# Kernel tuning notes

Hardware: AMD Instinct MI355X
Metric: run time of the kernel (lower is better)

Reference implementation:

```python
import jax, jax.numpy as jnp
import numpy as np

N_S, N_D, E, L = 10000, 2000, 100000, 50000
H = 8            # attention heads
H1, H2, H3 = 128, 128, 64
D_S, D_D = 128, 64
NEG_SLOPE = 0.2  # GATv2 leaky_relu slope


def setup_inputs() -> dict:
    key = jax.random.key(0)
    ks = iter(jax.random.split(key, 48))
    def nrm(shape, fan_in):
        return (jax.random.normal(next(ks), shape) / np.sqrt(fan_in)).astype(jnp.float32)
    inp = {}
    inp["x_snorna"] = jax.random.normal(next(ks), (N_S, D_S), dtype=jnp.float32)
    inp["x_disease"] = jax.random.normal(next(ks), (N_D, D_D), dtype=jnp.float32)
    inp["edge_src"] = jax.random.randint(next(ks), (E,), 0, N_S, dtype=jnp.int32)
    inp["edge_dst"] = jax.random.randint(next(ks), (E,), 0, N_D, dtype=jnp.int32)
    inp["edge_label_src"] = jax.random.randint(next(ks), (L,), 0, N_S, dtype=jnp.int32)
    inp["edge_label_dst"] = jax.random.randint(next(ks), (L,), 0, N_D, dtype=jnp.int32)
    # layer 1: GraphConv per relation (lin_rel has bias, lin_root no bias)
    inp["W1_rel_sd"] = nrm((D_S, H1), D_S); inp["b1_sd"] = jnp.zeros((H1,), jnp.float32)
    inp["W1_root_sd"] = nrm((D_D, H1), D_D)
    inp["W1_rel_ds"] = nrm((D_D, H1), D_D); inp["b1_ds"] = jnp.zeros((H1,), jnp.float32)
    inp["W1_root_ds"] = nrm((D_S, H1), D_S)
    # layer 2: GATv2Conv per relation (lin_l/lin_r with bias, att, final bias)
    for rel in ("sd", "ds"):
        inp[f"Wl2_{rel}"] = nrm((H1, H * H2), H1); inp[f"bl2_{rel}"] = jnp.zeros((H * H2,), jnp.float32)
        inp[f"Wr2_{rel}"] = nrm((H1, H * H2), H1); inp[f"br2_{rel}"] = jnp.zeros((H * H2,), jnp.float32)
        inp[f"att2_{rel}"] = nrm((H, H2), H2)
        inp[f"bias2_{rel}"] = jnp.zeros((H2,), jnp.float32)
    # layer 3: GraphConv per relation
    inp["W3_rel_sd"] = nrm((H2, H3), H2); inp["b3_sd"] = jnp.zeros((H3,), jnp.float32)
    inp["W3_root_sd"] = nrm((H2, H3), H2)
    inp["W3_rel_ds"] = nrm((H2, H3), H2); inp["b3_ds"] = jnp.zeros((H3,), jnp.float32)
    inp["W3_root_ds"] = nrm((H2, H3), H2)
    return inp


def graph_conv(x_src, x_dst, es, ed, W_rel, b_rel, W_root, n_dst):
    # PyG GraphConv: lin_rel(sum-aggregated neighbor feats) + lin_root(x_dst)
    agg = jax.ops.segment_sum(x_src[es], ed, num_segments=n_dst)
    return agg @ W_rel + b_rel + x_dst @ W_root


def gatv2(x_src, x_dst, es, ed, Wl, bl, Wr, br, att, bias, n_dst):
    # PyG GATv2Conv, bipartite, add_self_loops=False, concat=False (mean over heads)
    xl = (x_src @ Wl + bl).reshape(x_src.shape[0], H, -1)  # [Ns,H,C]
    xr = (x_dst @ Wr + br).reshape(x_dst.shape[0], H, -1)  # [Nd,H,C]
    xj = xl[es]                                            # [E,H,C] source msgs
    e = jax.nn.leaky_relu(xj + xr[ed], NEG_SLOPE)          # [E,H,C]
    score = jnp.einsum('ehc,hc->eh', e, att)               # [E,H]
    m = jax.ops.segment_max(score, ed, num_segments=n_dst)
    a = jnp.exp(score - m[ed])
    denom = jax.ops.segment_sum(a, ed, num_segments=n_dst)
    alpha = a / denom[ed]                                  # softmax over in-edges of dst
    out = jax.ops.segment_sum(alpha[:, :, None] * xj, ed, num_segments=n_dst)
    return out.mean(axis=1) + bias                         # concat=False -> head mean


def reference(x_snorna, x_disease, edge_src, edge_dst, edge_label_src, edge_label_dst,
              W1_rel_sd, b1_sd, W1_root_sd, W1_rel_ds, b1_ds, W1_root_ds,
              Wl2_sd, bl2_sd, Wr2_sd, br2_sd, att2_sd, bias2_sd,
              Wl2_ds, bl2_ds, Wr2_ds, br2_ds, att2_ds, bias2_ds,
              W3_rel_sd, b3_sd, W3_root_sd, W3_rel_ds, b3_ds, W3_root_ds):
    # HeteroConv layer 1 (GraphConv both directions); each type has one incoming relation
    xd = graph_conv(x_snorna, x_disease, edge_src, edge_dst, W1_rel_sd, b1_sd, W1_root_sd, N_D)
    xs = graph_conv(x_disease, x_snorna, edge_dst, edge_src, W1_rel_ds, b1_ds, W1_root_ds, N_S)
    xs, xd = jax.nn.relu(xs), jax.nn.relu(xd)  # dropout = identity (eval mode)
    # HeteroConv layer 2 (GATv2Conv both directions)
    xd2 = gatv2(xs, xd, edge_src, edge_dst, Wl2_sd, bl2_sd, Wr2_sd, br2_sd, att2_sd, bias2_sd, N_D)
    xs2 = gatv2(xd, xs, edge_dst, edge_src, Wl2_ds, bl2_ds, Wr2_ds, br2_ds, att2_ds, bias2_ds, N_S)
    xs2, xd2 = jax.nn.relu(xs2), jax.nn.relu(xd2)
    # HeteroConv layer 3 (GraphConv, no activation)
    xd3 = graph_conv(xs2, xd2, edge_src, edge_dst, W3_rel_sd, b3_sd, W3_root_sd, N_D)
    xs3 = graph_conv(xd2, xs2, edge_dst, edge_src, W3_rel_ds, b3_ds, W3_root_ds, N_S)
    # Classifier: per-pair dot product
    return (xs3[edge_label_src] * xd3[edge_label_dst]).sum(axis=-1)
```

## Files before the change

### kernel.cpp

```cpp
#include <hip/hip_runtime.h>
#include <math.h>

#define NEG 0.2f
static const int N_S = 10000, N_D = 2000, E_N = 100000, L_N = 50000;

using short8 = __attribute__((ext_vector_type(8))) short;
using f32x4  = __attribute__((ext_vector_type(4))) float;
typedef _Float16 h2 __attribute__((ext_vector_type(2)));

union U8h { uint4 u[2]; h2 h[8]; unsigned w[8]; };

__device__ inline unsigned short f2bf(float f) {
  unsigned u = __float_as_uint(f);
  u += 0x7fff + ((u >> 16) & 1);
  return (unsigned short)(u >> 16);
}
__device__ inline float bf2f(unsigned short u) {
  return __uint_as_float((unsigned)u << 16);
}
__device__ inline unsigned short f2h(float f) {
  _Float16 h = (_Float16)f;
  unsigned short r;
  __builtin_memcpy(&r, &h, 2);
  return r;
}

struct PkD { const float* W; unsigned short* P; int K, M; };
struct Pk12 { PkD d[12]; };
struct PrepArgs {
  const int *es, *ed;
  int *deg_s, *deg_d;
  const float *xs, *xd;
  unsigned short *xsb, *xdb;
  const float *att_sd, *att_ds;
  unsigned short *att16;
};
__global__ void k_prep(PrepArgs a, Pk12 g) {
  int bid = blockIdx.x, t = threadIdx.x;
  if (bid < 391) {
    int e = bid * 256 + t;
    if (e < E_N) {
      atomicAdd(&a.deg_d[a.ed[e]], 1);
      atomicAdd(&a.deg_s[a.es[e]], 1);
    }
  } else if (bid < 391 + 1375) {
    int i = (bid - 391) * 256 + t;
    const int ns4 = N_S * 32;
    if (i < ns4) {
      float4 v = ((const float4*)a.xs)[i];
      ushort4 o = {f2bf(v.x), f2bf(v.y), f2bf(v.z), f2bf(v.w)};
      ((ushort4*)a.xsb)[i] = o;
    } else {
      int j = i - ns4;
      float4 v = ((const float4*)a.xd)[j];
      ushort4 o = {f2bf(v.x), f2bf(v.y), f2bf(v.z), f2bf(v.w)};
      ((ushort4*)a.xdb)[j] = o;
    }
  } else if (bid < 391 + 1375 + 768) {
    int sub = bid - 391 - 1375;
    PkD d = g.d[sub >> 6];
    int total = d.K * d.M, mt = d.M >> 4;
    for (int tid = (sub & 63) * 256 + t; tid < total; tid += 64 * 256) {
      int r = tid & 7, l = (tid >> 3) & 63, rest = tid >> 9;
      int ct = rest % mt, kt = rest / mt;
      d.P[tid] = f2bf(d.W[(kt * 32 + (l >> 4) * 8 + r) * d.M + ct * 16 + (l & 15)]);
    }
  } else {
    int i = (bid - 391 - 1375 - 768) * 256 + t;
    float v = (i < 1024) ? a.att_sd[i] : a.att_ds[i - 1024];
    a.att16[i] = f2h(v);
  }
}

__global__ __launch_bounds__(1024) void k_scan2(int* c0, int* r0, int n0,
                                                int* c1, int* r1, int n1) {
  int* cur = blockIdx.x ? c1 : c0;
  int* rp  = blockIdx.x ? r1 : r0;
  int N    = blockIdx.x ? n1 : n0;
  __shared__ int wsum[16];
  __shared__ int carry;
  if (threadIdx.x == 0) carry = 0;
  __syncthreads();
  int lane = threadIdx.x & 63, wid = threadIdx.x >> 6;
  for (int base = 0; base < N; base += 1024) {
    int i = base + threadIdx.x;
    int v = (i < N) ? cur[i] : 0;
    int x = v;
    #pragma unroll
    for (int dd = 1; dd < 64; dd <<= 1) {
      int t = __shfl_up(x, dd);
      if (lane >= dd) x += t;
    }
    if (lane == 63) wsum[wid] = x;
    __syncthreads();
    int woff = 0;
    for (int ww = 0; ww < wid; ++ww) woff += wsum[ww];
    int excl = carry + woff + x - v;
    if (i < N) { rp[i] = excl; cur[i] = excl; }
    __syncthreads();
    if (threadIdx.x == 0) {
      int t = 0;
      #pragma unroll
      for (int ww = 0; ww < 16; ++ww) t += wsum[ww];
      if (base + 1024 >= N) rp[N] = carry + t;
      carry += t;
    }
    __syncthreads();
  }
}

__global__ void k_scat2(const int* __restrict__ es, const int* __restrict__ ed,
                        int* __restrict__ cur_d, int* __restrict__ cur_s,
                        int* __restrict__ csrc_d, int* __restrict__ csrc_s, int E) {
  int e = blockIdx.x * 256 + threadIdx.x;
  if (e >= E) return;
  int s = es[e], d = ed[e];
  csrc_d[atomicAdd(&cur_d[d], 1)] = s;
  csrc_s[atomicAdd(&cur_s[s], 1)] = d;
}

__device__ __forceinline__ void gath128(const unsigned short* __restrict__ x,
                                        const int* __restrict__ rp, const int* __restrict__ cs,
                                        unsigned short* __restrict__ out,
                                        int n, int half, int cl) {
  int b = rp[n], e = rp[n + 1];
  float a0 = 0.f, a1 = 0.f, a2 = 0.f, a3 = 0.f;
  int i = b + half;
  for (; i + 2 < e; i += 4) {
    uint2 v0 = *(const uint2*)(x + (long long)cs[i] * 128 + cl * 4);
    uint2 v1 = *(const uint2*)(x + (long long)cs[i + 2] * 128 + cl * 4);
    a0 += bf2f((unsigned short)(v0.x & 0xffff)) + bf2f((unsigned short)(v1.x & 0xffff));
    a1 += bf2f((unsigned short)(v0.x >> 16))    + bf2f((unsigned short)(v1.x >> 16));
    a2 += bf2f((unsigned short)(v0.y & 0xffff)) + bf2f((unsigned short)(v1.y & 0xffff));
    a3 += bf2f((unsigned short)(v0.y >> 16))    + bf2f((unsigned short)(v1.y >> 16));
  }
  for (; i < e; i += 2) {
    uint2 v0 = *(const uint2*)(x + (long long)cs[i] * 128 + cl * 4);
    a0 += bf2f((unsigned short)(v0.x & 0xffff));
    a1 += bf2f((unsigned short)(v0.x >> 16));
    a2 += bf2f((unsigned short)(v0.y & 0xffff));
    a3 += bf2f((unsigned short)(v0.y >> 16));
  }
  a0 += __shfl_xor(a0, 32); a1 += __shfl_xor(a1, 32);
  a2 += __shfl_xor(a2, 32); a3 += __shfl_xor(a3, 32);
  if (!half) {
    ushort4 o = {f2bf(a0), f2bf(a1), f2bf(a2), f2bf(a3)};
    *(ushort4*)&out[(long long)n * 128 + cl * 4] = o;
  }
}

__global__ __launch_bounds__(256) void k_gather1(
    const unsigned short* __restrict__ xsb, const unsigned short* __restrict__ xdb,
    const int* __restrict__ rpd, const int* __restrict__ csd,
    const int* __restrict__ rps, const int* __restrict__ css,
    unsigned short* __restrict__ aggd, unsigned short* __restrict__ aggs) {
  int wv = threadIdx.x >> 6, l = threadIdx.x & 63, half = l >> 5, cl = l & 31;
  int r = blockIdx.x % 6, q = blockIdx.x / 6;
  if (r == 0) {
    gath128(xsb, rpd, csd, aggd, q * 4 + wv, half, cl);
  } else {
    int n = (q * 5 + (r - 1)) * 4 + wv;
    if (n >= N_S) return;
    int b = rps[n], e = rps[n + 1];
    float a0 = 0.f, a1 = 0.f;
    int i = b + half;
    for (; i + 2 < e; i += 4) {
      unsigned v0 = *(const unsigned*)(xdb + (long long)css[i] * 64 + cl * 2);
      unsigned v1 = *(const unsigned*)(xdb + (long long)css[i + 2] * 64 + cl * 2);
      a0 += bf2f((unsigned short)(v0 & 0xffff)) + bf2f((unsigned short)(v1 & 0xffff));
      a1 += bf2f((unsigned short)(v0 >> 16))    + bf2f((unsigned short)(v1 >> 16));
    }
    for (; i < e; i += 2) {
      unsigned v0 = *(const unsigned*)(xdb + (long long)css[i] * 64 + cl * 2);
      a0 += bf2f((unsigned short)(v0 & 0xffff));
      a1 += bf2f((unsigned short)(v0 >> 16));
    }
    a0 += __shfl_xor(a0, 32); a1 += __shfl_xor(a1, 32);
    if (!half) {
      ushort2 o = {f2bf(a0), f2bf(a1)};
      *(ushort2*)&aggs[(long long)n * 64 + cl * 2] = o;
    }
  }
}

__global__ __launch_bounds__(256) void k_gather3(
    const unsigned short* __restrict__ xs2b, const unsigned short* __restrict__ xd2b,
    const int* __restrict__ rpd, const int* __restrict__ csd,
    const int* __restrict__ rps, const int* __restrict__ css,
    unsigned short* __restrict__ aggd, unsigned short* __restrict__ aggs) {
  int wv = threadIdx.x >> 6, l = threadIdx.x & 63, half = l >> 5, cl = l & 31;
  int r = blockIdx.x % 6, q = blockIdx.x / 6;
  if (r == 0) {
    gath128(xs2b, rpd, csd, aggd, q * 4 + wv, half, cl);
  } else {
    int n = (q * 5 + (r - 1)) * 4 + wv;
    if (n >= N_S) return;
    gath128(xd2b, rps, css, aggs, n, half, cl);
  }
}

struct GD {
  const unsigned short *A0, *P0, *A1, *P1;
  const float* bias;
  void* out;
  int K0, K1, N, M, relu, outmode, y0;
};
template<int ND> struct GDs { GD d[ND]; };

template<int ND>
__global__ __launch_bounds__(256) void k_mfma(GDs<ND> g) {
  int by = blockIdx.y;
  int di = 0;
  #pragma unroll
  for (int i = 1; i < ND; ++i) if (by >= g.d[i].y0) di = i;
  GD d = g.d[di];
  int ytile = by - d.y0;
  int c0 = blockIdx.x * 64;
  if (c0 >= d.M) return;
  int w = threadIdx.x >> 6, l = threadIdx.x & 63;
  int r0 = ytile * 64 + w * 16;
  if (r0 >= d.N) return;
  int lg = l >> 4, lo = l & 15;
  f32x4 acc[4] = {};
  int arow = r0 + lo; arow = (arow < d.N) ? arow : (d.N - 1);
  int mt = d.M >> 4;
  int ct0 = c0 >> 4;
  const unsigned short* a0 = d.A0 + (long long)arow * d.K0 + lg * 8;
  for (int kt = 0; kt < (d.K0 >> 5); ++kt) {
    short8 a = *(const short8*)(a0 + kt * 32);
    #pragma unroll
    for (int ct = 0; ct < 4; ++ct) {
      short8 b = *(const short8*)(d.P0 + ((long long)(kt * mt + ct0 + ct) * 64 + l) * 8);
      acc[ct] = __builtin_amdgcn_mfma_f32_16x16x32_bf16(a, b, acc[ct], 0, 0, 0);
    }
  }
  if (d.K1) {
    const unsigned short* a1 = d.A1 + (long long)arow * d.K1 + lg * 8;
    for (int kt = 0; kt < (d.K1 >> 5); ++kt) {
      short8 a = *(const short8*)(a1 + kt * 32);
      #pragma unroll
      for (int ct = 0; ct < 4; ++ct) {
        short8 b = *(const short8*)(d.P1 + ((long long)(kt * mt + ct0 + ct) * 64 + l) * 8);
        acc[ct] = __builtin_amdgcn_mfma_f32_16x16x32_bf16(a, b, acc[ct], 0, 0, 0);
      }
    }
  }
  #pragma unroll
  for (int ct = 0; ct < 4; ++ct) {
    int col = c0 + ct * 16 + lo;
    float bv = d.bias[col];
    #pragma unroll
    for (int r = 0; r < 4; ++r) {
      int grow = r0 + lg * 4 + r;
      if (grow < d.N) {
        float v = acc[ct][r] + bv;
        if (d.relu) v = fmaxf(v, 0.f);
        if (d.outmode == 1)
          ((unsigned short*)d.out)[(long long)grow * d.M + col] = f2bf(v);
        else if (d.outmode == 2)
          ((unsigned short*)d.out)[(long long)grow * d.M + col] = f2h(v);
        else
          ((float*)d.out)[(long long)grow * d.M + col] = v;
      }
    }
  }
}

template<int WPN>
__device__ __forceinline__ void gat_node(
    const unsigned short* __restrict__ xl, const unsigned short* __restrict__ xr,
    const int* __restrict__ rowptr, const int* __restrict__ srcid,
    const unsigned short* __restrict__ att16, const float* __restrict__ bias,
    unsigned short* __restrict__ outb, int node, int wsub, int l,
    float (*lm)[8], float (*lss)[8], unsigned (*lacc)[8][64]) {
  int h = l >> 3, sub = l & 7;
  int cbase = h * 128 + sub * 16;
  U8h xr8, at8;
  { const uint4* p = (const uint4*)(xr + (long long)node * 1024 + cbase);
    xr8.u[0] = p[0]; xr8.u[1] = p[1]; }
  { const uint4* p = (const uint4*)(att16 + cbase);
    at8.u[0] = p[0]; at8.u[1] = p[1]; }
  const h2 neg2 = {(_Float16)NEG, (_Float16)NEG};
  float m = -INFINITY, s = 0.f;
  h2 acc2[8] = {};
  int b = rowptr[node], e = rowptr[node + 1];
  int deg = e - b;

  auto ldrow = [&](int idx, U8h& dst) {
    int ic = idx < e - 1 ? idx : e - 1;
    ic = ic > 0 ? ic : 0;
    const uint4* p = (const uint4*)(xl + (long long)srcid[ic] * 1024 + cbase);
    dst.u[0] = p[0]; dst.u[1] = p[1];
  };

  auto process = [&](U8h& x, bool valid) {
    float sc = 0.f;
    #pragma unroll
    for (int j = 0; j < 8; ++j) {
      h2 t = x.h[j] + xr8.h[j];
      h2 lk = __builtin_elementwise_max(t, t * neg2);
      sc = __builtin_amdgcn_fdot2(lk, at8.h[j], sc, false);
    }
    sc += __shfl_xor(sc, 1); sc += __shfl_xor(sc, 2); sc += __shfl_xor(sc, 4);
    if (valid && sc > m + 4.f) {
      float scl = __expf(m - sc);
      _Float16 sh = (_Float16)scl;
      h2 s2 = {sh, sh};
      #pragma unroll
      for (int j = 0; j < 8; ++j) acc2[j] *= s2;
      s *= scl; m = sc;
    }
    float a = __expf(sc - m);
    a = valid ? a : 0.f;
    s += a;
    _Float16 ah = (_Float16)(a * 0.00390625f);
    h2 a2 = {ah, ah};
    #pragma unroll
    for (int j = 0; j < 8; ++j) acc2[j] = __builtin_elementwise_fma(a2, x.h[j], acc2[j]);
  };

  int i = b + wsub;
  int nmine = (deg - wsub + WPN - 1) / WPN;
  if (nmine < 0) nmine = 0;
  int npairs = (nmine + 1) >> 1;
  U8h c, d;
  ldrow(i, c);
  ldrow(i + WPN, d);
  for (int it = 0; it < npairs; ++it) {
    int j = i + 2 * WPN;
    U8h n0, n1;
    ldrow(j, n0);
    ldrow(j + WPN, n1);
    process(c, i < e);
    process(d, i + WPN < e);
    c = n0; d = n1; i = j;
  }

  float val[16];
  if constexpr (WPN == 4) {
    if (sub == 0) { lm[wsub][h] = m; lss[wsub][h] = s; }
    U8h tmp;
    #pragma unroll
    for (int j = 0; j < 8; ++j) tmp.h[j] = acc2[j];
    #pragma unroll
    for (int j = 0; j < 8; ++j) lacc[wsub][j][l] = tmp.w[j];
    __syncthreads();
    if (wsub != 0) return;
    float M2 = fmaxf(fmaxf(lm[0][h], lm[1][h]), fmaxf(lm[2][h], lm[3][h]));
    float S = 0.f;
    #pragma unroll
    for (int j = 0; j < 16; ++j) val[j] = 0.f;
    #pragma unroll
    for (int w2 = 0; w2 < 4; ++w2) {
      float scw = (M2 == -INFINITY) ? 0.f : __expf(lm[w2][h] - M2);
      S = fmaf(scw, lss[w2][h], S);
      #pragma unroll
      for (int j = 0; j < 8; ++j) {
        unsigned uw = lacc[w2][j][l];
        h2 hv; __builtin_memcpy(&hv, &uw, 4);
        val[2 * j]     = fmaf(scw, (float)hv[0], val[2 * j]);
        val[2 * j + 1] = fmaf(scw, (float)hv[1], val[2 * j + 1]);
      }
    }
    float inv = (S > 0.f) ? 256.f / S : 0.f;
    #pragma unroll
    for (int j = 0; j < 16; ++j) val[j] *= inv;
  } else {
    float inv = (s > 0.f) ? 256.f / s : 0.f;
    #pragma unroll
    for (int j = 0; j < 8; ++j) {
      val[2 * j]     = (float)acc2[j][0] * inv;
      val[2 * j + 1] = (float)acc2[j][1] * inv;
    }
  }
  #pragma unroll
  for (int j = 0; j < 16; ++j) {
    val[j] += __shfl_xor(val[j], 8);
    val[j] += __shfl_xor(val[j], 16);
    val[j] += __shfl_xor(val[j], 32);
  }
  if (l < 8) {
    #pragma unroll
    for (int q = 0; q < 4; ++q) {
      float4 bq = *(const float4*)&bias[sub * 16 + q * 4];
      ushort4 o;
      o.x = f2bf(fmaxf(val[q * 4 + 0] * 0.125f + bq.x, 0.f));
      o.y = f2bf(fmaxf(val[q * 4 + 1] * 0.125f + bq.y, 0.f));
      o.z = f2bf(fmaxf(val[q * 4 + 2] * 0.125f + bq.z, 0.f));
      o.w = f2bf(fmaxf(val[q * 4 + 3] * 0.125f + bq.w, 0.f));
      *(ushort4*)&outb[(long long)node * 128 + sub * 16 + q * 4] = o;
    }
  }
}

__global__ __launch_bounds__(256) void k_gat_both(
    const unsigned short* __restrict__ XLsd, const unsigned short* __restrict__ XRsd,
    const int* __restrict__ rpd, const int* __restrict__ csd,
    const unsigned short* __restrict__ att_sd, const float* __restrict__ bias_sd,
    unsigned short* __restrict__ XD2b,
    const unsigned short* __restrict__ XLds, const unsigned short* __restrict__ XRds,
    const int* __restrict__ rps, const int* __restrict__ css,
    const unsigned short* __restrict__ att_ds, const float* __restrict__ bias_ds,
    unsigned short* __restrict__ XS2b) {
  __shared__ float lm[4][8], lss[4][8];
  __shared__ unsigned lacc[4][8][64];
  int widx = threadIdx.x >> 6, l = threadIdx.x & 63;
  int r = blockIdx.x % 9, q = blockIdx.x / 9;
  if (r < 4) {
    gat_node<4>(XLsd, XRsd, rpd, csd, att_sd, bias_sd, XD2b,
                q * 4 + r, widx, l, lm, lss, lacc);
  } else {
    int node = (q * 5 + (r - 4)) * 4 + widx;
    if (node < N_S)
      gat_node<1>(XLds, XRds, rps, css, att_ds, bias_ds, XS2b,
                  node, 0, l, lm, lss, lacc);
  }
}

__global__ void k_dot64(const float* __restrict__ xs, const float* __restrict__ xd,
                        const int* __restrict__ ls, const int* __restrict__ ld,
                        float* __restrict__ out, int L) {
  long long t = (long long)blockIdx.x * blockDim.x + threadIdx.x;
  int wave = (int)(t >> 6), lane = (int)(t & 63);
  int q = lane >> 4, sub = lane & 15;
  int eidx = wave * 4 + q;
  if (eidx >= L) return;
  const float4* a = (const float4*)(xs + (long long)ls[eidx] * 64);
  const float4* b = (const float4*)(xd + (long long)ld[eidx] * 64);
  float4 va = a[sub], vb = b[sub];
  float v = va.x * vb.x + va.y * vb.y + va.z * vb.z + va.w * vb.w;
  v += __shfl_xor(v, 1); v += __shfl_xor(v, 2);
  v += __shfl_xor(v, 4); v += __shfl_xor(v, 8);
  if (sub == 0) out[eidx] = v;
}

extern "C" void kernel_launch(void* const* d_in, const int* in_sizes, int n_in,
                              void* d_out, int out_size, void* d_ws, size_t ws_size,
                              hipStream_t stream) {
  const float* x_s = (const float*)d_in[0];
  const float* x_d = (const float*)d_in[1];
  const int* esrc = (const int*)d_in[2];
  const int* edst = (const int*)d_in[3];
  const int* lsrc = (const int*)d_in[4];
  const int* ldst = (const int*)d_in[5];
  const float* W1rel_sd  = (const float*)d_in[6];
  const float* b1_sd     = (const float*)d_in[7];
  const float* W1root_sd = (const float*)d_in[8];
  const float* W1rel_ds  = (const float*)d_in[9];
  const float* b1_ds     = (const float*)d_in[10];
  const float* W1root_ds = (const float*)d_in[11];
  const float *Wl2_sd = (const float*)d_in[12], *bl2_sd = (const float*)d_in[13],
              *Wr2_sd = (const float*)d_in[14], *br2_sd = (const float*)d_in[15],
              *att2_sd = (const float*)d_in[16], *bias2_sd = (const float*)d_in[17];
  const float *Wl2_ds = (const float*)d_in[18], *bl2_ds = (const float*)d_in[19],
              *Wr2_ds = (const float*)d_in[20], *br2_ds = (const float*)d_in[21],
              *att2_ds = (const float*)d_in[22], *bias2_ds = (const float*)d_in[23];
  const float *W3rel_sd = (const float*)d_in[24], *b3_sd = (const float*)d_in[25],
              *W3root_sd = (const float*)d_in[26];
  const float *W3rel_ds = (const float*)d_in[27], *b3_ds = (const float*)d_in[28],
              *W3root_ds = (const float*)d_in[29];
  float* out = (float*)d_out;

  float* w = (float*)d_ws;
  long long off = 0;
  auto alloc = [&](long long n) { float* p = w + off; off += (n + 63) & ~63LL; return p; };
  unsigned short* xsb   = (unsigned short*)alloc((long long)N_S * 64);
  unsigned short* xdb   = (unsigned short*)alloc((long long)N_D * 32);
  unsigned short* AGGDb = (unsigned short*)alloc((long long)N_D * 64);
  unsigned short* AGGSb = (unsigned short*)alloc((long long)N_S * 32);
  unsigned short* XS1b  = (unsigned short*)alloc((long long)N_S * 64);
  unsigned short* XD1b  = (unsigned short*)alloc((long long)N_D * 64);
  unsigned short* XLsd  = (unsigned short*)alloc((long long)N_S * 512);
  unsigned short* XRsd  = (unsigned short*)alloc((long long)N_D * 512);
  unsigned short* XLds  = (unsigned short*)alloc((long long)N_D * 512);
  unsigned short* XRds  = (unsigned short*)alloc((long long)N_S * 512);
  unsigned short* XS2b  = (unsigned short*)alloc((long long)N_S * 64);
  unsigned short* XD2b  = (unsigned short*)alloc((long long)N_D * 64);
  unsigned short* AGD3b = (unsigned short*)alloc((long long)N_D * 64);
  unsigned short* AGS3b = (unsigned short*)alloc((long long)N_S * 64);
  float* XS3 = alloc((long long)N_S * 64);
  float* XD3 = alloc((long long)N_D * 64);
  unsigned short* att16 = (unsigned short*)alloc(1024 + 64);
  unsigned short* pk[12];
  const int pksz[12] = {128 * 128, 64 * 128, 64 * 128, 128 * 128,
                        131072, 131072, 131072, 131072,
                        128 * 64, 128 * 64, 128 * 64, 128 * 64};
  for (int i = 0; i < 12; ++i) pk[i] = (unsigned short*)alloc(pksz[i] / 2 + 64);
  int* rowptr_d = (int*)alloc(N_D + 64);
  int* rowptr_s = (int*)alloc(N_S + 64);
  int* cur_all  = (int*)alloc(N_D + N_S + 128);
  int* cur_d = cur_all;
  int* cur_s = cur_all + N_D + 64;
  int* csrc_d = (int*)alloc(E_N);
  int* csrc_s = (int*)alloc(E_N);
  (void)ws_size; (void)in_sizes; (void)n_in; (void)out_size;

  hipMemsetAsync(cur_all, 0, (size_t)(N_D + N_S + 128) * 4, stream);
  PrepArgs pa = {esrc, edst, cur_s, cur_d, x_s, x_d, xsb, xdb, att2_sd, att2_ds, att16};
  Pk12 pkk = {{{W1rel_sd, pk[0], 128, 128}, {W1root_sd, pk[1], 64, 128},
               {W1rel_ds, pk[2], 64, 128},  {W1root_ds, pk[3], 128, 128},
               {Wl2_sd, pk[4], 128, 1024},  {Wr2_sd, pk[5], 128, 1024},
               {Wl2_ds, pk[6], 128, 1024},  {Wr2_ds, pk[7], 128, 1024},
               {W3rel_sd, pk[8], 128, 64},  {W3root_sd, pk[9], 128, 64},
               {W3rel_ds, pk[10], 128, 64}, {W3root_ds, pk[11], 128, 64}}};
  k_prep<<<2542, 256, 0, stream>>>(pa, pkk);
  k_scan2<<<2, 1024, 0, stream>>>(cur_d, rowptr_d, N_D, cur_s, rowptr_s, N_S);
  k_scat2<<<391, 256, 0, stream>>>(esrc, edst, cur_d, cur_s, csrc_d, csrc_s, E_N);

  k_gather1<<<3000, 256, 0, stream>>>(xsb, xdb, rowptr_d, csrc_d, rowptr_s, csrc_s,
                                      AGGDb, AGGSb);
  {
    GDs<2> g = {{{AGGDb, pk[0], xdb, pk[1], b1_sd, XD1b, 128, 64, N_D, 128, 1, 1, 0},
                 {AGGSb, pk[2], xsb, pk[3], b1_ds, XS1b, 64, 128, N_S, 128, 1, 1, 32}}};
    k_mfma<2><<<dim3(2, 189), 256, 0, stream>>>(g);
  }

  {
    GDs<4> g = {{{XS1b, pk[4], nullptr, nullptr, bl2_sd, XLsd, 128, 0, N_S, 1024, 0, 2, 0},
                 {XD1b, pk[5], nullptr, nullptr, br2_sd, XRsd, 128, 0, N_D, 1024, 0, 2, 157},
                 {XD1b, pk[6], nullptr, nullptr, bl2_ds, XLds, 128, 0, N_D, 1024, 0, 2, 189},
                 {XS1b, pk[7], nullptr, nullptr, br2_ds, XRds, 128, 0, N_S, 1024, 0, 2, 221}}};
    k_mfma<4><<<dim3(16, 378), 256, 0, stream>>>(g);
  }
  k_gat_both<<<4500, 256, 0, stream>>>(
      XLsd, XRsd, rowptr_d, csrc_d, att16, bias2_sd, XD2b,
      XLds, XRds, rowptr_s, csrc_s, att16 + 1024, bias2_ds, XS2b);

  k_gather3<<<3000, 256, 0, stream>>>(XS2b, XD2b, rowptr_d, csrc_d, rowptr_s, csrc_s,
                                      AGD3b, AGS3b);
  {
    GDs<2> g = {{{AGD3b, pk[8], XD2b, pk[9], b3_sd, XD3, 128, 128, N_D, 64, 0, 0, 0},
                 {AGS3b, pk[10], XS2b, pk[11], b3_ds, XS3, 128, 128, N_S, 64, 0, 0, 32}}};
    k_mfma<2><<<dim3(1, 189), 256, 0, stream>>>(g);
  }

  k_dot64<<<(L_N * 16 + 255) / 256, 256, 0, stream>>>(XS3, XD3, lsrc, ldst, out, L_N);
}
```

Before: 198.9 us.

## Project layer-3 features before aggregation and triple-buffer GAT edge loads

New measurement: 207.6 us. +4.4%, slower.

```diff
diff --git a/kernel.cpp b/kernel.cpp
--- a/kernel.cpp
+++ b/kernel.cpp
@@ -23,6 +23,12 @@
   unsigned short r;
   __builtin_memcpy(&r, &h, 2);
   return r;
+}
+__device__ inline float h2lo(unsigned u) {
+  h2 v; __builtin_memcpy(&v, &u, 4); return (float)v[0];
+}
+__device__ inline float h2hi(unsigned u) {
+  h2 v; __builtin_memcpy(&v, &u, 4); return (float)v[1];
 }
 
 struct PkD { const float* W; unsigned short* P; int K, M; };
@@ -34,6 +40,7 @@
   unsigned short *xsb, *xdb;
   const float *att_sd, *att_ds;
   unsigned short *att16;
+  float *zbias;
 };
 __global__ void k_prep(PrepArgs a, Pk12 g) {
   int bid = blockIdx.x, t = threadIdx.x;
@@ -67,8 +74,12 @@
     }
   } else {
     int i = (bid - 391 - 1375 - 768) * 256 + t;
-    float v = (i < 1024) ? a.att_sd[i] : a.att_ds[i - 1024];
-    a.att16[i] = f2h(v);
+    if (i < 2048) {
+      float v = (i < 1024) ? a.att_sd[i] : a.att_ds[i - 1024];
+      a.att16[i] = f2h(v);
+    } else if (i < 2112) {
+      a.zbias[i - 2048] = 0.f;
+    }
   }
 }
 
@@ -113,6 +124,7 @@
                         int* __restrict__ cur_d, int* __restrict__ cur_s,
                         int* __restrict__ csrc_d, int* __restrict__ csrc_s, int E) {
   int e = blockIdx.x * 256 + threadIdx.x;
+  if (e < 64) { csrc_d[E + e] = 0; csrc_s[E + e] = 0; }
   if (e >= E) return;
   int s = es[e], d = ed[e];
   csrc_d[atomicAdd(&cur_d[d], 1)] = s;
@@ -184,18 +196,41 @@
 }
 
 __global__ __launch_bounds__(256) void k_gather3(
-    const unsigned short* __restrict__ xs2b, const unsigned short* __restrict__ xd2b,
+    const unsigned short* __restrict__ XPs, const unsigned short* __restrict__ XPd,
+    const float* __restrict__ ROOTd, const float* __restrict__ ROOTs,
     const int* __restrict__ rpd, const int* __restrict__ csd,
     const int* __restrict__ rps, const int* __restrict__ css,
-    unsigned short* __restrict__ aggd, unsigned short* __restrict__ aggs) {
+    float* __restrict__ XD3, float* __restrict__ XS3) {
   int wv = threadIdx.x >> 6, l = threadIdx.x & 63, half = l >> 5, cl = l & 31;
   int r = blockIdx.x % 6, q = blockIdx.x / 6;
+  const unsigned short* xp; const float* root; float* out;
+  const int *rp, *cs; int n;
   if (r == 0) {
-    gath128(xs2b, rpd, csd, aggd, q * 4 + wv, half, cl);
+    n = q * 4 + wv; xp = XPs; root = ROOTd; out = XD3; rp = rpd; cs = csd;
   } else {
-    int n = (q * 5 + (r - 1)) * 4 + wv;
+    n = (q * 5 + (r - 1)) * 4 + wv;
     if (n >= N_S) return;
-    gath128(xd2b, rps, css, aggs, n, half, cl);
+    xp = XPd; root = ROOTs; out = XS3; rp = rps; cs = css;
+  }
+  int b = rp[n], e = rp[n + 1];
+  float a0 = 0.f, a1 = 0.f;
+  int i = b + half;
+  for (; i + 2 < e; i += 4) {
+    unsigned v0 = *(const unsigned*)(xp + (long long)cs[i] * 64 + cl * 2);
+    unsigned v1 = *(const unsigned*)(xp + (long long)cs[i + 2] * 64 + cl * 2);
+    a0 += h2lo(v0) + h2lo(v1);
+    a1 += h2hi(v0) + h2hi(v1);
+  }
+  for (; i < e; i += 2) {
+    unsigned v0 = *(const unsigned*)(xp + (long long)cs[i] * 64 + cl * 2);
+    a0 += h2lo(v0);
+    a1 += h2hi(v0);
+  }
+  a0 += __shfl_xor(a0, 32); a1 += __shfl_xor(a1, 32);
+  if (!half) {
+    float2 rt = *(const float2*)&root[(long long)n * 64 + cl * 2];
+    float2 o = {a0 + rt.x, a1 + rt.y};
+    *(float2*)&out[(long long)n * 64 + cl * 2] = o;
   }
 }
 
@@ -287,9 +322,7 @@
   int deg = e - b;
 
   auto ldrow = [&](int idx, U8h& dst) {
-    int ic = idx < e - 1 ? idx : e - 1;
-    ic = ic > 0 ? ic : 0;
-    const uint4* p = (const uint4*)(xl + (long long)srcid[ic] * 1024 + cbase);
+    const uint4* p = (const uint4*)(xl + (long long)srcid[idx] * 1024 + cbase);
     dst.u[0] = p[0]; dst.u[1] = p[1];
   };
 
@@ -320,20 +353,19 @@
   };
 
   int i = b + wsub;
-  int nmine = (deg - wsub + WPN - 1) / WPN;
-  if (nmine < 0) nmine = 0;
-  int npairs = (nmine + 1) >> 1;
-  U8h c, d;
-  ldrow(i, c);
-  ldrow(i + WPN, d);
-  for (int it = 0; it < npairs; ++it) {
-    int j = i + 2 * WPN;
-    U8h n0, n1;
-    ldrow(j, n0);
-    ldrow(j + WPN, n1);
-    process(c, i < e);
-    process(d, i + WPN < e);
-    c = n0; d = n1; i = j;
+  int nmine = (deg > wsub) ? (deg - wsub + WPN - 1) / WPN : 0;
+  int ntrip = (nmine + 2) / 3;
+  U8h A, B, C;
+  ldrow(i, A);
+  ldrow(i + WPN, B);
+  for (int it = 0; it < ntrip; ++it) {
+    ldrow(i + 2 * WPN, C);
+    process(A, i < e);
+    ldrow(i + 3 * WPN, A);
+    process(B, i + WPN < e);
+    ldrow(i + 4 * WPN, B);
+    process(C, i + 2 * WPN < e);
+    i += 3 * WPN;
   }
 
   float val[16];
@@ -476,11 +508,14 @@
   unsigned short* XRds  = (unsigned short*)alloc((long long)N_S * 512);
   unsigned short* XS2b  = (unsigned short*)alloc((long long)N_S * 64);
   unsigned short* XD2b  = (unsigned short*)alloc((long long)N_D * 64);
-  unsigned short* AGD3b = (unsigned short*)alloc((long long)N_D * 64);
-  unsigned short* AGS3b = (unsigned short*)alloc((long long)N_S * 64);
+  unsigned short* XPs   = (unsigned short*)alloc((long long)N_S * 32);
+  unsigned short* XPd   = (unsigned short*)alloc((long long)N_D * 32);
+  float* ROOTd = alloc((long long)N_D * 64);
+  float* ROOTs = alloc((long long)N_S * 64);
   float* XS3 = alloc((long long)N_S * 64);
   float* XD3 = alloc((long long)N_D * 64);
   unsigned short* att16 = (unsigned short*)alloc(1024 + 64);
+  float* zbias = alloc(64);
   unsigned short* pk[12];
   const int pksz[12] = {128 * 128, 64 * 128, 64 * 128, 128 * 128,
                         131072, 131072, 131072, 131072,
@@ -491,19 +526,20 @@
   int* cur_all  = (int*)alloc(N_D + N_S + 128);
   int* cur_d = cur_all;
   int* cur_s = cur_all + N_D + 64;
-  int* csrc_d = (int*)alloc(E_N);
-  int* csrc_s = (int*)alloc(E_N);
+  int* csrc_d = (int*)alloc(E_N + 64);
+  int* csrc_s = (int*)alloc(E_N + 64);
   (void)ws_size; (void)in_sizes; (void)n_in; (void)out_size;
 
   hipMemsetAsync(cur_all, 0, (size_t)(N_D + N_S + 128) * 4, stream);
-  PrepArgs pa = {esrc, edst, cur_s, cur_d, x_s, x_d, xsb, xdb, att2_sd, att2_ds, att16};
+  PrepArgs pa = {esrc, edst, cur_s, cur_d, x_s, x_d, xsb, xdb,
+                 att2_sd, att2_ds, att16, zbias};
   Pk12 pkk = {{{W1rel_sd, pk[0], 128, 128}, {W1root_sd, pk[1], 64, 128},
                {W1rel_ds, pk[2], 64, 128},  {W1root_ds, pk[3], 128, 128},
                {Wl2_sd, pk[4], 128, 1024},  {Wr2_sd, pk[5], 128, 1024},
                {Wl2_ds, pk[6], 128, 1024},  {Wr2_ds, pk[7], 128, 1024},
                {W3rel_sd, pk[8], 128, 64},  {W3root_sd, pk[9], 128, 64},
                {W3rel_ds, pk[10], 128, 64}, {W3root_ds, pk[11], 128, 64}}};
-  k_prep<<<2542, 256, 0, stream>>>(pa, pkk);
+  k_prep<<<2543, 256, 0, stream>>>(pa, pkk);
   k_scan2<<<2, 1024, 0, stream>>>(cur_d, rowptr_d, N_D, cur_s, rowptr_s, N_S);
   k_scat2<<<391, 256, 0, stream>>>(esrc, edst, cur_d, cur_s, csrc_d, csrc_s, E_N);
 
@@ -526,13 +562,15 @@
       XLsd, XRsd, rowptr_d, csrc_d, att16, bias2_sd, XD2b,
       XLds, XRds, rowptr_s, csrc_s, att16 + 1024, bias2_ds, XS2b);
 
-  k_gather3<<<3000, 256, 0, stream>>>(XS2b, XD2b, rowptr_d, csrc_d, rowptr_s, csrc_s,
-                                      AGD3b, AGS3b);
   {
-    GDs<2> g = {{{AGD3b, pk[8], XD2b, pk[9], b3_sd, XD3, 128, 128, N_D, 64, 0, 0, 0},
-                 {AGS3b, pk[10], XS2b, pk[11], b3_ds, XS3, 128, 128, N_S, 64, 0, 0, 32}}};
-    k_mfma<2><<<dim3(1, 189), 256, 0, stream>>>(g);
-  }
+    GDs<4> g = {{{XS2b, pk[8],  nullptr, nullptr, zbias, XPs,   128, 0, N_S, 64, 0, 2, 0},
+                 {XD2b, pk[10], nullptr, nullptr, zbias, XPd,   128, 0, N_D, 64, 0, 2, 157},
+                 {XD2b, pk[9],  nullptr, nullptr, b3_sd, ROOTd, 128, 0, N_D, 64, 0, 0, 189},
+                 {XS2b, pk[11], nullptr, nullptr, b3_ds, ROOTs, 128, 0, N_S, 64, 0, 0, 221}}};
+    k_mfma<4><<<dim3(1, 378), 256, 0, stream>>>(g);
+  }
+  k_gather3<<<3000, 256, 0, stream>>>(XPs, XPd, ROOTd, ROOTs,
+                                      rowptr_d, csrc_d, rowptr_s, csrc_s, XD3, XS3);
 
   k_dot64<<<(L_N * 16 + 255) / 256, 256, 0, stream>>>(XS3, XD3, lsrc, ldst, out, L_N);
 }
```
